# Kernel tuning notes

Measured on AMD Instinct MI355X. Metric: run time of the kernel, lower is better.

Reference implementation:

```python
import jax, jax.numpy as jnp
import numpy as np

N_NODES, NUM_FEAT, EMB, HID, N_CLASSES, N_EDGES = 800, 111, 32, 200, 15, 8000
ALPHA = 0.5   # DirGNNConv default mixing
EPS = 1e-5    # LayerNorm eps


def _pade_coeffs(deg=5):
    # [5/5] Pade approximant of sqrt(1 - x) (as in FastDifferentiableMatSqrt)
    K = 2 * deg + 1
    b = np.zeros(K); b[0] = 1.0
    for k in range(1, K):
        b[k] = b[k - 1] * (0.5 - (k - 1)) / k
    c = b * ((-1.0) ** np.arange(K))  # Taylor coeffs of sqrt(1-x)
    A = np.empty((deg, deg))
    for i in range(deg):
        for j in range(1, deg + 1):
            A[i, j - 1] = c[deg + 1 + i - j]
    q = np.concatenate([[1.0], np.linalg.solve(A, -c[deg + 1:])])
    p = np.array([sum(q[j] * c[k - j] for j in range(min(k, deg) + 1)) for k in range(deg + 1)])
    return p.astype(np.float32), q.astype(np.float32)

PADE_P, PADE_Q = _pade_coeffs()


def _mpa_impl(A):
    # matrix square root via Pade approximant (MPA forward)
    normA = jnp.sqrt(jnp.sum(A * A))
    I = jnp.eye(A.shape[0], dtype=A.dtype)
    p_app = I - A / normA
    p_hat = p_app
    p_sqrt = PADE_P[0] * I
    q_sqrt = PADE_Q[0] * I
    for i in range(5):
        p_sqrt = p_sqrt + PADE_P[i + 1] * p_hat
        q_sqrt = q_sqrt + PADE_Q[i + 1] * p_hat
        p_hat = p_hat @ p_app
    return jnp.linalg.solve(q_sqrt, p_sqrt) * jnp.sqrt(normA)


@jax.custom_vjp
def mpa_lya(A):
    return _mpa_impl(A)


def _mpa_fwd(A):
    S = _mpa_impl(A)
    return S, (S, jnp.sqrt(jnp.sum(A * A)))


def _mpa_bwd(res, g):
    # iterative Lyapunov solver backward (8 coupled Newton-Schulz iterations)
    S, normA = res
    I = jnp.eye(S.shape[0], dtype=S.dtype)
    b = S / jnp.sqrt(normA)
    c = g / jnp.sqrt(normA)
    for _ in range(8):
        b2 = b @ b
        c = 0.5 * (c @ (3.0 * I - b2) - b2 @ c + b @ (c @ b))
        b = 0.5 * (b @ (3.0 * I - b2))
    return (0.5 * c,)

mpa_lya.defvjp(_mpa_fwd, _mpa_bwd)


def gcn_sparse(m, ei, n):
    # GCNConv(normalize=False): out[dst] = sum_{(src,dst) in E} (x @ W)[src]
    return jax.ops.segment_sum(m[ei[0]], ei[1], num_segments=n)


def hetero_layer_sparse(h, eis, W, b):
    # W: [3(in,out,root), 4 edge types, Fin, Fout]; HeteroConv aggr='sum'
    n = h.shape[0]
    out = jnp.zeros((n, W.shape[-1]), h.dtype)
    for e, ei in enumerate(eis):
        x_in = gcn_sparse(h @ W[0, e], ei, n) + b[0, e]
        x_out = gcn_sparse(h @ W[1, e], ei[::-1], n) + b[1, e]  # flipped edges
        out = out + ALPHA * x_out + (1.0 - ALPHA) * x_in + h @ W[2, e] + b[2, e]
    return out


def hetero_layer_dense(h, masks, W, b):
    # masks: [4, N, N] binary adjacency (src, dst); dense equivalent of scatter
    out = jnp.zeros((h.shape[0], W.shape[-1]), h.dtype)
    for e in range(masks.shape[0]):
        x_in = masks[e].T @ (h @ W[0, e]) + b[0, e]
        x_out = masks[e] @ (h @ W[1, e]) + b[1, e]
        out = out + ALPHA * x_out + (1.0 - ALPHA) * x_in + h @ W[2, e] + b[2, e]
    return out


def graph_layernorm(h, wb):
    # PyG LayerNorm mode='graph', single graph: normalize over all nodes+feats
    mu = jnp.mean(h)
    var = jnp.mean((h - mu) ** 2)
    return (h - mu) / jnp.sqrt(var + EPS) * wb[0] + wb[1]


def hetero_gnn(h, layer_fn, graph, W1, b1, W2, b2, ln):
    h = graph_layernorm(layer_fn(h, graph, W1, b1), ln[0])
    return graph_layernorm(layer_fn(h, graph, W2, b2), ln[1])


def pairwise_S(z, lin_W, lin_b, iu, ju):
    n = z.shape[0]
    M = (z[iu] - z[ju]) ** 2                        # [N(N+1)/2, HID]
    mg = jax.nn.sigmoid(M @ lin_W + lin_b)[:, 0]    # upper-tri entries, row-major
    tri = jnp.zeros((n, n), z.dtype).at[iu, ju].set(mg)
    return mpa_lya(tri)


def model_forward(x_note, embed_W, embed_b, g1_l1_W, g1_l1_b, g1_l2_W, g1_l2_b, g1_ln,
                  g2_l1_W, g2_l1_b, g2_l2_W, g2_l2_b, g2_ln, lin_W, lin_b, clf_W, clf_b,
                  eis, batch):
    n = x_note.shape[0]
    iu, ju = np.triu_indices(n)
    h = x_note @ embed_W + embed_b                   # [N, 32]
    z0 = hetero_gnn(h, hetero_layer_sparse, eis, g1_l1_W, g1_l1_b, g1_l2_W, g1_l2_b, g1_ln)
    S1 = pairwise_S(z0, lin_W, lin_b, iu, ju)
    A0 = jnp.stack([jnp.zeros((n, n), h.dtype).at[ei[0], ei[1]].set(1.0) for ei in eis])
    h = S1 @ h
    # adj_to_coord(nonzero) only keeps the binary pattern of S1 @ A @ S1
    mask1 = jnp.stack([((S1 @ A0[e]) @ S1 != 0).astype(h.dtype) for e in range(4)])
    z1 = hetero_gnn(h, hetero_layer_dense, mask1, g2_l1_W, g2_l1_b, g2_l2_W, g2_l2_b, g2_ln)
    S2 = pairwise_S(z1, lin_W, lin_b, iu, ju)
    h = S2 @ h
    mask2 = jnp.stack([((S2 @ mask1[e]) @ S2 != 0).astype(h.dtype) for e in range(4)])
    z2 = hetero_gnn(h, hetero_layer_dense, mask2, g2_l1_W, g2_l1_b, g2_l2_W, g2_l2_b, g2_ln)
    counts = jax.ops.segment_sum(jnp.ones((n,), z2.dtype), batch, num_segments=1)
    x2 = jax.ops.segment_sum(z2, batch, num_segments=1) / counts[:, None]  # global_mean_pool
    logits = x2 @ clf_W + clf_b
    return x2, jax.nn.log_softmax(logits, axis=-1), S1, S2


def setup_inputs() -> dict:
    key = jax.random.key(0)
    ks = jax.random.split(key, 14)
    N, F, E, H, NC, NE = N_NODES, NUM_FEAT, EMB, HID, N_CLASSES, N_EDGES
    def w(k, shape, fan_in):
        return (jax.random.normal(k, shape, jnp.float32) / np.sqrt(fan_in)).astype(jnp.float32)
    ln = jnp.broadcast_to(jnp.stack([jnp.ones(H, jnp.float32), jnp.zeros(H, jnp.float32)]), (2, 2, H)) + 0.0
    return dict(
        x_note=jax.random.normal(ks[0], (N, F), jnp.float32),
        embed_W=w(ks[1], (F, E), F), embed_b=jnp.zeros((E,), jnp.float32),
        g1_l1_W=w(ks[2], (3, 4, E, H), E), g1_l1_b=jnp.zeros((3, 4, H), jnp.float32),
        g1_l2_W=w(ks[3], (3, 4, H, H), H), g1_l2_b=jnp.zeros((3, 4, H), jnp.float32),
        g1_ln=ln,
        g2_l1_W=w(ks[4], (3, 4, E, H), E), g2_l1_b=jnp.zeros((3, 4, H), jnp.float32),
        g2_l2_W=w(ks[5], (3, 4, H, H), H), g2_l2_b=jnp.zeros((3, 4, H), jnp.float32),
        g2_ln=ln,
        lin_W=w(ks[6], (H, 1), H), lin_b=jnp.zeros((1,), jnp.float32),
        clf_W=w(ks[7], (H, NC), H), clf_b=jnp.zeros((NC,), jnp.float32),
        ei_forward=jax.random.randint(ks[8], (2, NE), 0, N, jnp.int32),
        ei_onset=jax.random.randint(ks[9], (2, NE), 0, N, jnp.int32),
        ei_sustain=jax.random.randint(ks[10], (2, NE), 0, N, jnp.int32),
        ei_rest=jax.random.randint(ks[11], (2, NE), 0, N, jnp.int32),
        batch=jnp.zeros((N,), jnp.int32),
    )


def reference(x_note, embed_W, embed_b, g1_l1_W, g1_l1_b, g1_l2_W, g1_l2_b, g1_ln,
              g2_l1_W, g2_l1_b, g2_l2_W, g2_l2_b, g2_ln, lin_W, lin_b, clf_W, clf_b,
              ei_forward, ei_onset, ei_sustain, ei_rest, batch):
    eis = (ei_forward, ei_onset, ei_sustain, ei_rest)
    return model_forward(x_note, embed_W, embed_b, g1_l1_W, g1_l1_b, g1_l2_W, g1_l2_b, g1_ln,
                         g2_l1_W, g2_l1_b, g2_l2_W, g2_l2_b, g2_ln, lin_W, lin_b, clf_W, clf_b,
                         eis, batch)
```

## Files before the change

### kernel.cpp

```cpp
#include <hip/hip_runtime.h>
#include <hip/hip_bf16.h>
#include <math.h>
#include <stdio.h>

static constexpr int   kN  = 800;
static constexpr int   kF  = 111;
static constexpr int   kE  = 32;
static constexpr int   kH  = 200;
static constexpr int   kNC = 15;
static constexpr int   kNE = 8000;
static constexpr long  kNN = (long)kN*kN;
static constexpr long  kNH = (long)kN*kH;
static constexpr float kAl  = 0.5f;
static constexpr float kEps = 1e-5f;
static constexpr int   kGB  = (int)((kNH+255)/256);
static constexpr int   kDB  = 50;

typedef unsigned short u16;
typedef __attribute__((ext_vector_type(8))) short short8;
typedef __attribute__((ext_vector_type(4))) float f32x4;

__device__ __forceinline__ u16 f2bf(float v){
  __hip_bfloat16 b = __float2bfloat16(v);
  return *reinterpret_cast<u16*>(&b);
}
__device__ __forceinline__ float bf2f(u16 h){
  unsigned int u = ((unsigned int)h) << 16;
  float f; __builtin_memcpy(&f, &u, 4);
  return f;
}

enum { EPI_NONE=0, EPI_BIAS=1, EPI_SCALE=4, EPI_ACC=6 };

template<bool TRANSA, bool TRIUA, bool TRIUB, int EPI, bool LNA>
__global__ __launch_bounds__(256)
void gemm_kernel(const float* __restrict__ A, int lda,
                 const float* __restrict__ B, int ldb,
                 float* __restrict__ C, int ldc,
                 int M, int Ncl, int K,
                 long sA, long sB, long sC, float scale,
                 const float* __restrict__ bias, int kstep,
                 const double* __restrict__ scalp,
                 const float* __restrict__ lnw,
                 const double* __restrict__ lnpart, int lnnb)
{
  constexpr int TM=64, TN=64, TK=16;
  A += (long)blockIdx.z * sA;
  B += (long)blockIdx.z * sB;
  C += (long)blockIdx.z * sC;
  __shared__ float As[TK][TM+4];
  __shared__ float Bs[TK][TN+4];
  const int tid = threadIdx.x;
  const int tn4 = (tid & 15)*4, tm4 = (tid >> 4)*4;
  const int m0 = blockIdx.x * TM, n0 = blockIdx.y * TN;
  float acc[4][4] = {};
  float mu = 0.f, rsf = 1.f;
  if (LNA){
    __shared__ double lnS[256], lnQ[256];
    double s=0.0, q=0.0;
    for (int i=tid; i<lnnb; i+=256){ s += lnpart[2*i]; q += lnpart[2*i+1]; }
    lnS[tid]=s; lnQ[tid]=q;
    __syncthreads();
    for (int h=128; h>0; h>>=1){
      if (tid < h){ lnS[tid]+=lnS[tid+h]; lnQ[tid]+=lnQ[tid+h]; }
      __syncthreads();
    }
    double m = lnS[0]/(double)kNH;
    double var = lnQ[0]/(double)kNH - m*m;
    mu = (float)m;
    rsf = rsqrtf((float)var + kEps);
    __syncthreads();
  }
  const int kbase = kstep ? (int)blockIdx.z * kstep : 0;
  int k0 = TRIUA ? max(m0 - kbase, 0) : 0;
  int kEnd = TRIUB ? min(K, n0 + TN - kbase) : K;
  const bool skip = (k0 >= kEnd);
  if (skip && EPI == EPI_ACC) return;
  if (!skip) {
    float ar[4], br[4];
    auto loadT = [&](int kk0, float* arr, float* brr){
      #pragma unroll
      for (int u=0; u<4; ++u){
        int idx = tid + 256*u;
        float av = 0.f;
        if (!TRANSA) {
          int m = idx >> 4, ka = idx & 15;
          int gm = m0+m, gk = kk0+ka;
          if (gm < M && gk < K){
            av = A[(long)gm*lda + gk];
            if (LNA) av = (av - mu)*(rsf*lnw[gk]) + lnw[kH + gk];
          }
        } else {
          int ka = idx >> 6, m = idx & 63;
          int gm = m0+m, gk = kk0+ka;
          if (gm < M && gk < K){
            av = A[(long)gk*lda + gm];
            if (LNA) av = (av - mu)*(rsf*lnw[gk]) + lnw[kH + gk];
          }
        }
        int kb = idx >> 6, nb = idx & 63;
        int gk = kk0+kb, gn = n0+nb;
        arr[u] = av;
        brr[u] = (gk < K && gn < Ncl) ? B[(long)gk*ldb + gn] : 0.f;
      }
    };
    auto storeT = [&](const float* arr, const float* brr){
      #pragma unroll
      for (int u=0; u<4; ++u){
        int idx = tid + 256*u;
        if (!TRANSA){ int m = idx>>4, ka = idx&15; As[ka][m] = arr[u]; }
        else        { int ka = idx>>6, m = idx&63; As[ka][m] = arr[u]; }
        int kb = idx>>6, nb = idx&63;
        Bs[kb][nb] = brr[u];
      }
    };
    loadT(k0, ar, br);
    for (;;){
      __syncthreads();
      storeT(ar, br);
      __syncthreads();
      int kn = k0 + TK;
      bool more = kn < kEnd;
      if (more) loadT(kn, ar, br);
      #pragma unroll
      for (int kk=0; kk<TK; ++kk) {
        float a[4], b[4];
        #pragma unroll
        for (int u=0;u<4;++u){ a[u]=As[kk][tm4+u]; b[u]=Bs[kk][tn4+u]; }
        #pragma unroll
        for (int i=0;i<4;++i)
          #pragma unroll
          for (int j=0;j<4;++j)
            acc[i][j] = fmaf(a[i], b[j], acc[i][j]);
      }
      if (!more) break;
      k0 = kn;
    }
  }
  float sc = scale;
  if (EPI == EPI_ACC && scalp) sc *= (float)sqrt(sqrt(scalp[0]));
  #pragma unroll
  for (int i=0;i<4;++i) {
    int gm = m0 + tm4 + i;
    if (gm >= M) continue;
    #pragma unroll
    for (int j=0;j<4;++j) {
      int gn = n0 + tn4 + j;
      if (gn >= Ncl) continue;
      float v = acc[i][j];
      long off = (long)gm*ldc + gn;
      if (EPI == EPI_BIAS)       C[off] = v + bias[gn];
      else if (EPI == EPI_SCALE) C[off] = scale*v;
      else if (EPI == EPI_ACC)   unsafeAtomicAdd(&C[off], sc*v);
      else                       C[off] = v;
    }
  }
}

template<bool TRANSA, bool TRIUA, bool TRIUB, int EPI, bool LNA = false>
static inline void launch_gemm(hipStream_t st,
                               const float* A, int lda, const float* B, int ldb,
                               float* C, int ldc, int M, int Ncl, int K, int batch,
                               long sA, long sB, long sC, float scale,
                               const float* bias = nullptr, int kstep = 0,
                               const double* scalp = nullptr,
                               const float* lnw = nullptr,
                               const double* lnpart = nullptr, int lnnb = 0)
{
  dim3 grid((M+63)/64, (Ncl+63)/64, batch);
  gemm_kernel<TRANSA,TRIUA,TRIUB,EPI,LNA><<<grid, 256, 0, st>>>(
      A,lda,B,ldb,C,ldc,M,Ncl,K,sA,sB,sC,scale,bias,kstep,scalp,lnw,lnpart,lnnb);
}

__global__ __launch_bounds__(256)
void bgemm2_kernel(const u16* __restrict__ Ah, const u16* __restrict__ Al,
                   const u16* __restrict__ Bh, const u16* __restrict__ Bl,
                   float* __restrict__ C, float* __restrict__ C2,
                   u16* __restrict__ Oh, u16* __restrict__ Ol,
                   float p0, float p1)
{
  constexpr int TM=64, TN=64, BK=32;
  __shared__ u16 Ash[TM][40], Asl[TM][40], Bsh[TN][40], Bsl[TN][40];
  const int tid = threadIdx.x;
  const int m0 = blockIdx.x*TM, n0 = blockIdx.y*TN;
  const int w = tid>>6, lane = tid&63;
  const int wm = (w&1)*32, wn = (w>>1)*32;
  const int quad = lane>>4, lm = lane&15;
  f32x4 acc00={}, acc01={}, acc10={}, acc11={};
  const bool skip = (m0 > n0 + TN - 1);
  int k0 = m0;
  const int kEnd = min(kN, n0+TN);
  const int ar = tid>>2, ac = (tid&3)*8;
  if (!skip){
    uint4 avh, avl, bvh, bvl;
    auto loadT = [&](int kk0){
      avh = {0,0,0,0}; avl = {0,0,0,0}; bvh = {0,0,0,0}; bvl = {0,0,0,0};
      int gk = kk0 + ac;
      if (m0+ar < kN && gk < kN){
        avh = *(const uint4*)(Ah + (long)(m0+ar)*kN + gk);
        avl = *(const uint4*)(Al + (long)(m0+ar)*kN + gk);
      }
      if (n0+ar < kN && gk < kN){
        bvh = *(const uint4*)(Bh + (long)(n0+ar)*kN + gk);
        bvl = *(const uint4*)(Bl + (long)(n0+ar)*kN + gk);
      }
    };
    loadT(k0);
    for (;;){
      __syncthreads();
      *(uint4*)&Ash[ar][ac] = avh; *(uint4*)&Asl[ar][ac] = avl;
      *(uint4*)&Bsh[ar][ac] = bvh; *(uint4*)&Bsl[ar][ac] = bvl;
      __syncthreads();
      int kn = k0 + BK;
      bool more = kn < kEnd;
      if (more) loadT(kn);
      short8 a0h = *(const short8*)&Ash[wm+lm][quad*8];
      short8 a1h = *(const short8*)&Ash[wm+16+lm][quad*8];
      short8 a0l = *(const short8*)&Asl[wm+lm][quad*8];
      short8 a1l = *(const short8*)&Asl[wm+16+lm][quad*8];
      short8 b0h = *(const short8*)&Bsh[wn+lm][quad*8];
      short8 b1h = *(const short8*)&Bsh[wn+16+lm][quad*8];
      short8 b0l = *(const short8*)&Bsl[wn+lm][quad*8];
      short8 b1l = *(const short8*)&Bsl[wn+16+lm][quad*8];
      acc00 = __builtin_amdgcn_mfma_f32_16x16x32_bf16(a0h,b0h,acc00,0,0,0);
      acc00 = __builtin_amdgcn_mfma_f32_16x16x32_bf16(a0h,b0l,acc00,0,0,0);
      acc00 = __builtin_amdgcn_mfma_f32_16x16x32_bf16(a0l,b0h,acc00,0,0,0);
      acc01 = __builtin_amdgcn_mfma_f32_16x16x32_bf16(a0h,b1h,acc01,0,0,0);
      acc01 = __builtin_amdgcn_mfma_f32_16x16x32_bf16(a0h,b1l,acc01,0,0,0);
      acc01 = __builtin_amdgcn_mfma_f32_16x16x32_bf16(a0l,b1h,acc01,0,0,0);
      acc10 = __builtin_amdgcn_mfma_f32_16x16x32_bf16(a1h,b0h,acc10,0,0,0);
      acc10 = __builtin_amdgcn_mfma_f32_16x16x32_bf16(a1h,b0l,acc10,0,0,0);
      acc10 = __builtin_amdgcn_mfma_f32_16x16x32_bf16(a1l,b0h,acc10,0,0,0);
      acc11 = __builtin_amdgcn_mfma_f32_16x16x32_bf16(a1h,b1h,acc11,0,0,0);
      acc11 = __builtin_amdgcn_mfma_f32_16x16x32_bf16(a1h,b1l,acc11,0,0,0);
      acc11 = __builtin_amdgcn_mfma_f32_16x16x32_bf16(a1l,b1h,acc11,0,0,0);
      if (!more) break;
      k0 = kn;
    }
  }
  f32x4 accs[2][2] = {{acc00, acc01},{acc10, acc11}};
  #pragma unroll
  for (int ti=0; ti<2; ++ti){
    #pragma unroll
    for (int tj=0; tj<2; ++tj){
      #pragma unroll
      for (int r=0; r<4; ++r){
        int gm = m0 + wm + ti*16 + quad*4 + r;
        int gn = n0 + wn + tj*16 + lm;
        if (gm >= kN || gn >= kN) continue;
        float v = accs[ti][tj][r];
        long off = (long)gm*kN + gn;
        C[off]  += p0*v;
        C2[off] += p1*v;
        u16 h = f2bf(v);
        Oh[off] = h;
        Ol[off] = f2bf(v - bf2f(h));
      }
    }
  }
}

__global__ __launch_bounds__(256)
void ln_pair_prep_kernel(const float* __restrict__ tnh, const double* __restrict__ part,
                         int nb, const float* __restrict__ ln, const float* __restrict__ linW,
                         u16* __restrict__ zwh, u16* __restrict__ zwl,
                         u16* __restrict__ zzh, u16* __restrict__ zzl,
                         float* __restrict__ avec)
{
  __shared__ double ss[256], qq[256];
  __shared__ float ared[256];
  const int n = blockIdx.x, t = threadIdx.x;
  double s=0.0, q=0.0;
  for (int i=t; i<nb; i+=256){ s += part[2*i]; q += part[2*i+1]; }
  ss[t]=s; qq[t]=q;
  __syncthreads();
  for (int h=128; h>0; h>>=1){
    if (t < h){ ss[t]+=ss[t+h]; qq[t]+=qq[t+h]; }
    __syncthreads();
  }
  double m = ss[0]/(double)kNH;
  const float mu = (float)m;
  const float rs = rsqrtf((float)(qq[0]/(double)kNH - m*m) + kEps);
  float acc = 0.f;
  if (t < kH){
    float z = (tnh[(long)n*kH + t] - mu)*(rs*ln[t]) + ln[kH + t];
    float wv = linW[t];
    float zw = wv*z;
    long off = (long)n*kH + t;
    u16 h1 = f2bf(zw);
    zwh[off] = h1; zwl[off] = f2bf(zw - bf2f(h1));
    u16 h2 = f2bf(z);
    zzh[off] = h2; zzl[off] = f2bf(z - bf2f(h2));
    acc = zw*z;
  }
  ared[t] = acc;
  __syncthreads();
  for (int h=128; h>0; h>>=1){
    if (t < h) ared[t] += ared[t+h];
    __syncthreads();
  }
  if (t == 0) avec[n] = ared[0];
}

__global__ __launch_bounds__(256)
void bgemm_pair_kernel(const u16* __restrict__ Ah, const u16* __restrict__ Al,
                       const u16* __restrict__ Bh, const u16* __restrict__ Bl,
                       const float* __restrict__ avec, const float* __restrict__ linb,
                       float* __restrict__ tri, double* __restrict__ frob2)
{
  constexpr int TM=64, TN=64, BK=32, KK=kH;
  __shared__ u16 Ash[TM][40], Asl[TM][40], Bsh[TN][40], Bsl[TN][40];
  __shared__ float red[256];
  const int tid = threadIdx.x;
  const int m0 = blockIdx.x*TM, n0 = blockIdx.y*TN;
  if (m0 > n0 + TN - 1){
    for (int idx = tid; idx < TM*TN; idx += 256){
      int r = idx >> 6, c = idx & 63;
      int gm = m0 + r, gn = n0 + c;
      if (gm < kN && gn < kN) tri[(long)gm*kN + gn] = 0.f;
    }
    return;
  }
  const int w = tid>>6, lane = tid&63;
  const int wm = (w&1)*32, wn = (w>>1)*32;
  const int quad = lane>>4, lm = lane&15;
  f32x4 acc00={}, acc01={}, acc10={}, acc11={};
  const int ar = tid>>2, ac = (tid&3)*8;
  for (int k0 = 0; k0 < KK; k0 += BK){
    uint4 avh={0,0,0,0}, avl={0,0,0,0}, bvh={0,0,0,0}, bvl={0,0,0,0};
    int gk = k0 + ac;
    if (m0+ar < kN && gk < KK){
      avh = *(const uint4*)(Ah + (long)(m0+ar)*KK + gk);
      avl = *(const uint4*)(Al + (long)(m0+ar)*KK + gk);
    }
    if (n0+ar < kN && gk < KK){
      bvh = *(const uint4*)(Bh + (long)(n0+ar)*KK + gk);
      bvl = *(const uint4*)(Bl + (long)(n0+ar)*KK + gk);
    }
    __syncthreads();
    *(uint4*)&Ash[ar][ac] = avh; *(uint4*)&Asl[ar][ac] = avl;
    *(uint4*)&Bsh[ar][ac] = bvh; *(uint4*)&Bsl[ar][ac] = bvl;
    __syncthreads();
    short8 a0h = *(const short8*)&Ash[wm+lm][quad*8];
    short8 a1h = *(const short8*)&Ash[wm+16+lm][quad*8];
    short8 a0l = *(const short8*)&Asl[wm+lm][quad*8];
    short8 a1l = *(const short8*)&Asl[wm+16+lm][quad*8];
    short8 b0h = *(const short8*)&Bsh[wn+lm][quad*8];
    short8 b1h = *(const short8*)&Bsh[wn+16+lm][quad*8];
    short8 b0l = *(const short8*)&Bsl[wn+lm][quad*8];
    short8 b1l = *(const short8*)&Bsl[wn+16+lm][quad*8];
    acc00 = __builtin_amdgcn_mfma_f32_16x16x32_bf16(a0h,b0h,acc00,0,0,0);
    acc00 = __builtin_amdgcn_mfma_f32_16x16x32_bf16(a0h,b0l,acc00,0,0,0);
    acc00 = __builtin_amdgcn_mfma_f32_16x16x32_bf16(a0l,b0h,acc00,0,0,0);
    acc01 = __builtin_amdgcn_mfma_f32_16x16x32_bf16(a0h,b1h,acc01,0,0,0);
    acc01 = __builtin_amdgcn_mfma_f32_16x16x32_bf16(a0h,b1l,acc01,0,0,0);
    acc01 = __builtin_amdgcn_mfma_f32_16x16x32_bf16(a0l,b1h,acc01,0,0,0);
    acc10 = __builtin_amdgcn_mfma_f32_16x16x32_bf16(a1h,b0h,acc10,0,0,0);
    acc10 = __builtin_amdgcn_mfma_f32_16x16x32_bf16(a1h,b0l,acc10,0,0,0);
    acc10 = __builtin_amdgcn_mfma_f32_16x16x32_bf16(a1l,b0h,acc10,0,0,0);
    acc11 = __builtin_amdgcn_mfma_f32_16x16x32_bf16(a1h,b1h,acc11,0,0,0);
    acc11 = __builtin_amdgcn_mfma_f32_16x16x32_bf16(a1h,b1l,acc11,0,0,0);
    acc11 = __builtin_amdgcn_mfma_f32_16x16x32_bf16(a1l,b1h,acc11,0,0,0);
  }
  const float lb = linb[0];
  float r2 = 0.f;
  f32x4 accs[2][2] = {{acc00, acc01},{acc10, acc11}};
  #pragma unroll
  for (int ti=0; ti<2; ++ti){
    #pragma unroll
    for (int tj=0; tj<2; ++tj){
      #pragma unroll
      for (int r=0; r<4; ++r){
        int gm = m0 + wm + ti*16 + quad*4 + r;
        int gn = n0 + wn + tj*16 + lm;
        if (gm >= kN || gn >= kN) continue;
        float t = 0.f;
        if (gm <= gn){
          float marg = avec[gm] + avec[gn] - 2.f*accs[ti][tj][r] + lb;
          t = 1.f/(1.f + expf(-marg));
        }
        tri[(long)gm*kN + gn] = t;
        r2 += t*t;
      }
    }
  }
  red[tid] = r2;
  __syncthreads();
  for (int h=128; h>0; h>>=1){
    if (tid < h) red[tid] += red[tid+h];
    __syncthreads();
  }
  if (tid == 0) unsafeAtomicAdd(frob2, (double)red[0]);
}

__global__ __launch_bounds__(256)
void pade_both_kernel(const float* __restrict__ tri, const double* __restrict__ frob2,
                      u16* __restrict__ ph, u16* __restrict__ pl,
                      u16* __restrict__ th, u16* __restrict__ tl,
                      float* __restrict__ psq, float* __restrict__ qsq,
                      float P0, float P1, float Q0, float Q1)
{
  __shared__ float t[32][33];
  const float rn = (float)(1.0 / sqrt(frob2[0]));
  int r0 = blockIdx.y*32, c0 = blockIdx.x*32;
  int tr = threadIdx.x>>5, tc = threadIdx.x&31;
  for (int i=tr; i<32; i+=8){
    int r = r0+i, c = c0+tc;
    float eye = (r==c) ? 1.f : 0.f;
    float pa = eye - tri[(long)r*kN + c]*rn;
    t[i][tc] = pa;
    long off = (long)r*kN + c;
    psq[off] = P0*eye + P1*pa;
    qsq[off] = Q0*eye + Q1*pa;
    u16 h = f2bf(pa);
    ph[off] = h;
    pl[off] = f2bf(pa - bf2f(h));
  }
  __syncthreads();
  for (int i=tr; i<32; i+=8){
    int c = c0+i, r = r0+tc;
    float v = t[tc][i];
    u16 h = f2bf(v);
    th[(long)c*kN + r] = h;
    tl[(long)c*kN + r] = f2bf(v - bf2f(h));
  }
}

__global__ __launch_bounds__(256)
void copy_scale_kernel(const float* __restrict__ src, const double* __restrict__ frob2,
                       float* __restrict__ dst)
{
  const float fac = (float)sqrt(sqrt(frob2[0]));
  long i = (long)blockIdx.x*256 + threadIdx.x;
  if (i < kNN) __builtin_nontemporal_store(src[i]*fac, &dst[i]);
}

__global__ void edge_count_kernel(const int* __restrict__ e0, const int* __restrict__ e1,
                                  const int* __restrict__ e2, const int* __restrict__ e3,
                                  int* __restrict__ cnt){
  const int* eis[4] = {e0,e1,e2,e3};
  const int e = blockIdx.y;
  const int* ei = eis[e];
  int j = blockIdx.x*256 + threadIdx.x;
  if (j >= kNE) return;
  int s = ei[j], d = ei[kNE + j];
  atomicAdd(&cnt[e*kN + d], 1);
  atomicAdd(&cnt[(4+e)*kN + s], 1);
}

__global__ void csr_scan_kernel(const int* __restrict__ cnt, int* __restrict__ offs,
                                int* __restrict__ cur){
  const int l = blockIdx.x;
  if (threadIdx.x != 0) return;
  int acc = 0;
  for (int i = 0; i < kN; ++i){
    offs[l*(kN+1) + i] = acc;
    cur[l*kN + i] = acc;
    acc += cnt[l*kN + i];
  }
  offs[l*(kN+1) + kN] = acc;
}

__global__ void edge_fill_kernel(const int* __restrict__ e0, const int* __restrict__ e1,
                                 const int* __restrict__ e2, const int* __restrict__ e3,
                                 int* __restrict__ cur, int* __restrict__ adj){
  const int* eis[4] = {e0,e1,e2,e3};
  const int e = blockIdx.y;
  const int* ei = eis[e];
  int j = blockIdx.x*256 + threadIdx.x;
  if (j >= kNE) return;
  int s = ei[j], d = ei[kNE + j];
  int p = atomicAdd(&cur[e*kN + d], 1);
  adj[(long)e*kNE + p] = s;
  int q = atomicAdd(&cur[(4+e)*kN + s], 1);
  adj[(long)(4+e)*kNE + q] = d;
}

__global__ __launch_bounds__(256)
void gather_sparse_kernel(const float* __restrict__ Y, const int* __restrict__ offs,
                          const int* __restrict__ adj, const float* __restrict__ bsum,
                          float* __restrict__ tnh, double* __restrict__ part){
  __shared__ double ss[256], qq[256];
  const int n = blockIdx.x;
  const int f = threadIdx.x;
  double sp = 0.0, qp = 0.0;
  float acc = 0.f;
  if (f < kH){
    #pragma unroll
    for (int l = 0; l < 8; ++l){
      const float* Yp = Y + (long)l*kNH;
      int b = offs[l*(kN+1) + n], e2 = offs[l*(kN+1) + n + 1];
      for (int idx = b; idx < e2; ++idx){
        int m = adj[(long)l*kNE + idx];
        acc += Yp[(long)m*kH + f];
      }
    }
    float t = Y[(long)8*kNH + (long)n*kH + f] + bsum[f] + 0.5f*acc;
    tnh[(long)n*kH + f] = t;
    sp = t; qp = (double)t*t;
  }
  ss[threadIdx.x]=sp; qq[threadIdx.x]=qp;
  __syncthreads();
  for (int hh=128; hh>0; hh>>=1){
    if ((int)threadIdx.x < hh){ ss[threadIdx.x]+=ss[threadIdx.x+hh]; qq[threadIdx.x]+=qq[threadIdx.x+hh]; }
    __syncthreads();
  }
  if (threadIdx.x==0){ part[2*blockIdx.x]=ss[0]; part[2*blockIdx.x+1]=qq[0]; }
}

__global__ void edge_gmax_kernel(const int* __restrict__ e0, const int* __restrict__ e1,
                                 const int* __restrict__ e2, const int* __restrict__ e3,
                                 int* __restrict__ g){
  const int* eis[4] = {e0,e1,e2,e3};
  const int e = blockIdx.y;
  const int* ei = eis[e];
  int j = blockIdx.x*256 + threadIdx.x;
  if (j >= kNE) return;
  int s = ei[j], d = ei[kNE + j];
  atomicMax(&g[e*kN + d], s);
}

__global__ __launch_bounds__(256)
void scan_gh_kernel(int* __restrict__ g, int* __restrict__ h){
  __shared__ int gs[kN];
  const int e = blockIdx.x;
  for (int i = threadIdx.x; i < kN; i += 256) gs[i] = g[e*kN + i];
  __syncthreads();
  if (threadIdx.x == 0){
    int m = -1;
    for (int i = 0; i < kN; ++i){ m = max(m, gs[i]); gs[i] = m; }
  }
  __syncthreads();
  for (int i = threadIdx.x; i < kN; i += 256) g[e*kN + i] = gs[i];
  for (int d = threadIdx.x; d < kN; d += 256){
    int lo = 0, hi = kN;
    while (lo < hi){ int mid = (lo+hi)>>1; if (gs[mid] >= d) hi = mid; else lo = mid+1; }
    h[e*kN + d] = lo;
  }
}

__global__ __launch_bounds__(256)
void scan_msg_kernel(float* __restrict__ Y){
  const int plane = blockIdx.x;
  const int f = threadIdx.x;
  if (f >= kH) return;
  float* P = Y + (long)plane*kNH + f;
  float acc = 0.f;
  if (plane < 4){
    for (int n = 0; n < kN; n += 4){
      float v0 = P[(long)(n+0)*kH], v1 = P[(long)(n+1)*kH];
      float v2 = P[(long)(n+2)*kH], v3 = P[(long)(n+3)*kH];
      acc += v0; P[(long)(n+0)*kH] = acc;
      acc += v1; P[(long)(n+1)*kH] = acc;
      acc += v2; P[(long)(n+2)*kH] = acc;
      acc += v3; P[(long)(n+3)*kH] = acc;
    }
  } else {
    for (int n = kN-1; n >= 0; n -= 4){
      float v0 = P[(long)(n-0)*kH], v1 = P[(long)(n-1)*kH];
      float v2 = P[(long)(n-2)*kH], v3 = P[(long)(n-3)*kH];
      acc += v0; P[(long)(n-0)*kH] = acc;
      acc += v1; P[(long)(n-1)*kH] = acc;
      acc += v2; P[(long)(n-2)*kH] = acc;
      acc += v3; P[(long)(n-3)*kH] = acc;
    }
  }
}

__global__ __launch_bounds__(256)
void gather_dense_kernel(const float* __restrict__ Y, const int* __restrict__ g,
                         const int* __restrict__ h, const float* __restrict__ bsum,
                         float* __restrict__ tnh, double* __restrict__ part){
  __shared__ double ss[256], qq[256];
  long idx = (long)blockIdx.x*256 + threadIdx.x;
  double s = 0.0, q = 0.0;
  if (idx < kNH){
    int n = (int)(idx / kH), f = (int)(idx % kH);
    float v = 0.f;
    #pragma unroll
    for (int e = 0; e < 4; ++e){
      int gi = g[e*kN + n];
      if (gi >= 0) v += Y[(long)e*kNH + (long)gi*kH + f];
      int hi = h[e*kN + n];
      if (hi < kN) v += Y[(long)(4+e)*kNH + (long)hi*kH + f];
    }
    float t = Y[(long)8*kNH + idx] + bsum[f] + 0.5f*v;
    tnh[idx] = t;
    s = t; q = (double)t*t;
  }
  ss[threadIdx.x]=s; qq[threadIdx.x]=q;
  __syncthreads();
  for (int hh=128; hh>0; hh>>=1){
    if ((int)threadIdx.x < hh){ ss[threadIdx.x]+=ss[threadIdx.x+hh]; qq[threadIdx.x]+=qq[threadIdx.x+hh]; }
    __syncthreads();
  }
  if (threadIdx.x==0){ part[2*blockIdx.x]=ss[0]; part[2*blockIdx.x+1]=qq[0]; }
}

__global__ void sum_root_kernel(const float* __restrict__ W, const float* __restrict__ b,
                                int K, float* __restrict__ Wr, float* __restrict__ bsum){
  int idx = blockIdx.x*256 + threadIdx.x;
  int tot = K*kH;
  if (idx < tot){
    float v = 0.f;
    #pragma unroll
    for (int e=0;e<4;++e) v += W[(long)(8+e)*tot + idx];
    Wr[idx] = v;
  }
  if (idx < kH){
    float v = 0.f;
    #pragma unroll
    for (int e=0;e<4;++e)
      v += (1.f-kAl)*b[(0*4+e)*kH + idx] + kAl*b[(1*4+e)*kH + idx] + b[(2*4+e)*kH + idx];
    bsum[idx] = v;
  }
}

__global__ __launch_bounds__(64)
void invdiag_kernel(const float* __restrict__ U, float* __restrict__ W){
  __shared__ float Us[kDB][kDB+1];
  __shared__ float Xs[kDB][kDB+1];
  const int base = blockIdx.x * kDB;
  const int tid = threadIdx.x;
  for (int idx = tid; idx < kDB*kDB; idx += 64){
    int r = idx / kDB, c = idx % kDB;
    Us[r][c] = U[(long)(base+r)*kN + base + c];
  }
  __syncthreads();
  const int c = tid;
  for (int i = kDB-1; i >= 0; --i){
    if (c < kDB){
      float x;
      if (c < i) x = 0.f;
      else {
        float s = 0.f;
        for (int k = i+1; k < kDB; ++k) s = fmaf(Us[i][k], Xs[k][c], s);
        x = (((c==i)?1.f:0.f) - s) / Us[i][i];
      }
      Xs[i][c] = x;
    }
    __syncthreads();
  }
  for (int idx = tid; idx < kDB*kDB; idx += 64){
    int r = idx / kDB, cc = idx % kDB;
    W[(long)(base+r)*kN + base + cc] = Xs[r][cc];
  }
}

template<int S>
__global__ __launch_bounds__(256)
void merge_fused_kernel(const float* __restrict__ U, float* __restrict__ W){
  __shared__ float Us[S][S+1];
  __shared__ float Wb[S][S+1];
  __shared__ float T[S][S+1];
  const long base = (long)blockIdx.x * (2*S) * (kN+1);
  const int tid = threadIdx.x;
  for (int idx = tid; idx < S*S; idx += 256){
    int r = idx / S, c = idx % S;
    Us[r][c] = U[base + (long)r*kN + S + c];
    Wb[r][c] = W[base + (long)(S+r)*kN + S + c];
  }
  __syncthreads();
  for (int idx = tid; idx < S*S; idx += 256){
    int r = idx / S, c = idx % S;
    float s = 0.f;
    for (int k = 0; k <= c; ++k) s = fmaf(Us[r][k], Wb[k][c], s);
    T[r][c] = s;
  }
  __syncthreads();
  for (int idx = tid; idx < S*S; idx += 256){
    int r = idx / S, c = idx % S;
    Us[r][c] = W[base + (long)r*kN + c];
  }
  __syncthreads();
  for (int idx = tid; idx < S*S; idx += 256){
    int r = idx / S, c = idx % S;
    float s = 0.f;
    for (int k = r; k < S; ++k) s = fmaf(Us[r][k], T[k][c], s);
    W[base + (long)r*kN + S + c] = -s;
  }
}

__global__ __launch_bounds__(256)
void pool_head_kernel(const float* __restrict__ z2raw, const double* __restrict__ part, int nb,
                      const float* __restrict__ ln,
                      const float* __restrict__ W, const float* __restrict__ b,
                      float* __restrict__ out){
  __shared__ double sred[256], qred[256];
  __shared__ float x2[kH];
  __shared__ float lg[kNC];
  int t = threadIdx.x;
  double s=0.0, q=0.0;
  for (int i=t; i<nb; i+=256){ s += part[2*i]; q += part[2*i+1]; }
  sred[t]=s; qred[t]=q;
  __syncthreads();
  for (int hh=128; hh>0; hh>>=1){
    if (t < hh){ sred[t]+=sred[t+hh]; qred[t]+=qred[t+hh]; }
    __syncthreads();
  }
  const float mu = (float)(sred[0] / (double)kNH);
  const float rs = rsqrtf((float)(qred[0]/(double)kNH - (sred[0]/(double)kNH)*(sred[0]/(double)kNH)) + kEps);
  if (t < kH){
    float sc = rs*ln[t], of = ln[kH+t];
    float sum = 0.f;
    for (int n = 0; n < kN; ++n) sum += (z2raw[(long)n*kH + t] - mu)*sc + of;
    float v = sum * (1.f/(float)kN);
    x2[t] = v;
    out[t] = v;
  }
  __syncthreads();
  if (t < kNC){
    float sv = b[t];
    for (int f = 0; f < kH; ++f) sv = fmaf(x2[f], W[f*kNC + t], sv);
    lg[t] = sv;
  }
  __syncthreads();
  if (t == 0){
    float m = -1e30f;
    for (int c=0;c<kNC;++c) m = fmaxf(m, lg[c]);
    float se = 0.f;
    for (int c=0;c<kNC;++c) se += expf(lg[c]-m);
    float lse = m + logf(se);
    for (int c=0;c<kNC;++c) out[kH + c] = lg[c]-lse;
  }
}

static void pade_coeffs(float* P, float* Q){
  double b[11]; b[0] = 1.0;
  for (int k=1;k<11;++k) b[k] = b[k-1]*(0.5-(k-1))/k;
  double c[11];
  for (int k=0;k<11;++k) c[k] = b[k]*((k&1)?-1.0:1.0);
  double A[5][5], rhs[5];
  for (int i=0;i<5;++i){ for (int j=0;j<5;++j) A[i][j] = c[5+i-j]; rhs[i] = -c[6+i]; }
  for (int col=0; col<5; ++col){
    int p = col;
    for (int r=col+1;r<5;++r) if (fabs(A[r][col]) > fabs(A[p][col])) p = r;
    if (p != col){
      for (int j=0;j<5;++j){ double t=A[col][j]; A[col][j]=A[p][j]; A[p][j]=t; }
      double t=rhs[col]; rhs[col]=rhs[p]; rhs[p]=t;
    }
    for (int r=col+1;r<5;++r){
      double f = A[r][col]/A[col][col];
      for (int j=col;j<5;++j) A[r][j] -= f*A[col][j];
      rhs[r] -= f*rhs[col];
    }
  }
  double q[6]; q[0] = 1.0;
  for (int r=4;r>=0;--r){
    double s = rhs[r];
    for (int j=r+1;j<5;++j) s -= A[r][j]*q[1+j];
    q[1+r] = s/A[r][r];
  }
  double p[6];
  for (int k=0;k<6;++k){
    double s = 0.0; int jm = k<5?k:5;
    for (int j=0;j<=jm;++j) s += q[j]*c[k-j];
    p[k] = s;
  }
  for (int k=0;k<6;++k){ P[k]=(float)p[k]; Q[k]=(float)q[k]; }
}

extern "C" void kernel_launch(void* const* d_in, const int* in_sizes, int n_in,
                              void* d_out, int out_size, void* d_ws, size_t ws_size,
                              hipStream_t stream)
{
  const float* x_note = (const float*)d_in[0];
  const float* embW   = (const float*)d_in[1];
  const float* embB   = (const float*)d_in[2];
  const float* g1w1   = (const float*)d_in[3];
  const float* g1b1   = (const float*)d_in[4];
  const float* g1w2   = (const float*)d_in[5];
  const float* g1b2   = (const float*)d_in[6];
  const float* g1ln   = (const float*)d_in[7];
  const float* g2w1   = (const float*)d_in[8];
  const float* g2b1   = (const float*)d_in[9];
  const float* g2w2   = (const float*)d_in[10];
  const float* g2b2   = (const float*)d_in[11];
  const float* g2ln   = (const float*)d_in[12];
  const float* linW   = (const float*)d_in[13];
  const float* linb   = (const float*)d_in[14];
  const float* clfW   = (const float*)d_in[15];
  const float* clfb   = (const float*)d_in[16];
  const int*  e0     = (const int*)d_in[17];
  const int*  e1     = (const int*)d_in[18];
  const int*  e2     = (const int*)d_in[19];
  const int*  e3     = (const int*)d_in[20];
  float* out = (float*)d_out;

  constexpr long o_h0   = 4096;
  constexpr long o_h1   = o_h0   + (long)kN*kE;
  constexpr long o_h2   = o_h1   + (long)kN*kE;
  constexpr long o_tnh  = o_h2   + (long)kN*kE;
  constexpr long o_pp   = o_tnh  + kNH;
  constexpr long o_av   = o_pp   + 2*kNH;
  constexpr long o_big  = o_av   + kN;
  constexpr long o_tri  = o_big  + 4*kNN;
  constexpr long o_sacc = o_tri  + kNN;
  constexpr long o_winv = o_sacc + kNN;
  constexpr long o_psq  = o_winv + kNN;
  constexpr long o_qsq  = o_psq  + kNN;
  constexpr long o_g    = o_qsq  + kNN;
  constexpr long o_hh   = o_g    + 4*kN;
  constexpr long o_wc1  = o_hh   + 4*kN;
  constexpr long o_wc2  = o_wc1  + 9L*kE*kH;
  constexpr long o_wc3  = o_wc2  + 9L*kH*kH;
  constexpr long o_wc4  = o_wc3  + 9L*kE*kH;
  constexpr long o_bs   = o_wc4  + 9L*kH*kH;
  constexpr long o_cnt  = o_bs   + 4*kH;
  constexpr long o_offs = o_cnt  + 8*kN;
  constexpr long o_cur  = o_offs + 8*(kN+1);
  constexpr long o_adj  = o_cur  + 8*kN;
  constexpr long o_end  = o_adj  + 8*(long)kNE;

  if (ws_size < (size_t)o_end*sizeof(float) || out_size < 215 + 2*(int)kNN || n_in < 21){
    fprintf(stderr, "kernel_launch guard: ws=%zu need=%zu out=%d need=%d n_in=%d\n",
            ws_size, (size_t)o_end*sizeof(float), out_size, (int)(215+2*kNN), n_in);
    hipMemsetAsync(d_out, 0, (size_t)out_size*sizeof(float), stream);
    return;
  }

  float* ws = (float*)d_ws;
  double* scald = (double*)d_ws;
  double* partd = (double*)((char*)d_ws + 512);
  float *h0=ws+o_h0, *h1=ws+o_h1, *h2=ws+o_h2, *tnh=ws+o_tnh,
        *big=ws+o_big, *tri=ws+o_tri, *Sacc=ws+o_sacc, *winv=ws+o_winv,
        *psq=ws+o_psq, *qsq=ws+o_qsq;
  u16* zwh = (u16*)(ws + o_pp);
  u16* zwl = zwh + kNH;
  u16* zzh = zwl + kNH;
  u16* zzl = zzh + kNH;
  float* avec = ws + o_av;
  int* gArr = (int*)(ws + o_g);
  int* hArr = (int*)(ws + o_hh);
  float *wc1=ws+o_wc1, *wc2=ws+o_wc2, *wc3=ws+o_wc3, *wc4=ws+o_wc4, *bs=ws+o_bs;
  int* cntA = (int*)(ws + o_cnt);
  int* offsA= (int*)(ws + o_offs);
  int* curA = (int*)(ws + o_cur);
  int* adjA = (int*)(ws + o_adj);
  u16* papp_h = (u16*)big;
  u16* papp_l = papp_h + kNN;
  u16* pT_h   = papp_l + kNN;
  u16* pT_l   = pT_h + kNN;
  u16* pwA_h  = pT_l + kNN;
  u16* pwA_l  = pwA_h + kNN;
  u16* pwB_h  = pwA_l + kNN;
  u16* pwB_l  = pwB_h + kNN;

  float P[6], Q[6];
  pade_coeffs(P, Q);

  auto eg = [](long n){ return dim3((unsigned)((n+255)/256)); };

  auto layer_gemm = [&](const float* hin, int K, const float* wcat,
                        const float* lnp, int nb){
    if (lnp)
      launch_gemm<false,false,false,EPI_NONE,true>(stream, hin, K, wcat, kH, big, kH,
          kN, kH, K, 9, 0, (long)K*kH, kNH, 0.f, nullptr, 0, nullptr, lnp, partd, nb);
    else
      launch_gemm<false,false,false,EPI_NONE>(stream, hin, K, wcat, kH, big, kH,
          kN, kH, K, 9, 0, (long)K*kH, kNH, 0.f);
  };
  auto sparse_layer = [&](const float* hin, int K, const float* wcat, const float* bsum,
                          const float* lnp, int nb){
    layer_gemm(hin, K, wcat, lnp, nb);
    gather_sparse_kernel<<<dim3(kN),256,0,stream>>>(big, offsA, adjA, bsum, tnh, partd);
  };
  auto dense_layer = [&](const float* hin, int K, const float* wcat, const float* bsum,
                         const float* lnp, int nb){
    layer_gemm(hin, K, wcat, lnp, nb);
    scan_msg_kernel<<<8,256,0,stream>>>(big);
    gather_dense_kernel<<<kGB,256,0,stream>>>(big, gArr, hArr, bsum, tnh, partd);
  };
  auto blocked_trsm = [&](){
    hipMemsetAsync(winv, 0, (size_t)kNN*sizeof(float), stream);
    invdiag_kernel<<<dim3(kN/kDB),64,0,stream>>>(qsq, winv);
    merge_fused_kernel<50><<<dim3(kN/100),256,0,stream>>>(qsq, winv);
    {
      int s = 100, npairs = 4;
      long step = (long)2*s*kN + 2*s;
      launch_gemm<false,false,true,EPI_NONE>(stream,
          qsq + s, kN, winv + (long)s*kN + s, kN, tri, s,
          s, s, s, npairs, step, step, (long)s*s, 0.f);
      launch_gemm<false,true,false,EPI_SCALE>(stream,
          winv, kN, tri, s, winv + s, kN,
          s, s, s, npairs, step, (long)s*s, step, -1.f);
    }
    {
      int s = 200, npairs = 2;
      long step = (long)2*s*kN + 2*s;
      launch_gemm<false,false,true,EPI_NONE>(stream,
          qsq + s, kN, winv + (long)s*kN + s, kN, tri, s,
          s, s, s, npairs, step, step, (long)s*s, 0.f);
      launch_gemm<false,true,false,EPI_SCALE>(stream,
          winv, kN, tri, s, winv + s, kN,
          s, s, s, npairs, step, (long)s*s, step, -1.f);
    }
    {
      hipMemsetAsync(tri, 0, (size_t)400*400*sizeof(float), stream);
      launch_gemm<false,false,true,EPI_ACC>(stream,
          qsq + 400, kN, winv + (long)400*kN + 400, kN, tri, 400,
          400, 400, 100, 4, 100, (long)100*kN, 0, 1.f, nullptr, 100);
      launch_gemm<false,true,false,EPI_ACC>(stream,
          winv, kN, tri, 400, winv + 400, kN,
          400, 400, 100, 4, 100, (long)100*400, 0, -1.f, nullptr, 100);
    }
    hipMemsetAsync(Sacc, 0, (size_t)kNN*sizeof(float), stream);
    launch_gemm<false,true,true,EPI_ACC>(stream,
        winv, kN, psq, kN, Sacc, kN, kN, kN, 100, 8,
        100, (long)100*kN, 0, 1.f, nullptr, 100);
  };
  auto run_pair_mpa = [&](int nb, const float* lnp, float* SoutDst){
    hipMemsetAsync((char*)d_ws + 24, 0, 8, stream);
    ln_pair_prep_kernel<<<dim3(kN),256,0,stream>>>(tnh, partd, nb, lnp, linW,
                                                   zwh, zwl, zzh, zzl, avec);
    bgemm_pair_kernel<<<dim3(13,13),256,0,stream>>>(zwh, zwl, zzh, zzl, avec, linb,
                                                    tri, scald+3);
    pade_both_kernel<<<dim3(25,25),256,0,stream>>>(tri, scald+3, papp_h, papp_l, pT_h, pT_l,
                                                   psq, qsq, P[0],P[1],Q[0],Q[1]);
    dim3 g13(13,13,1);
    bgemm2_kernel<<<g13,256,0,stream>>>(papp_h,papp_l, pT_h,pT_l, psq,qsq, pwA_h,pwA_l, P[2],Q[2]);
    bgemm2_kernel<<<g13,256,0,stream>>>(pwA_h,pwA_l,  pT_h,pT_l, psq,qsq, pwB_h,pwB_l, P[3],Q[3]);
    bgemm2_kernel<<<g13,256,0,stream>>>(pwB_h,pwB_l,  pT_h,pT_l, psq,qsq, pwA_h,pwA_l, P[4],Q[4]);
    bgemm2_kernel<<<g13,256,0,stream>>>(pwA_h,pwA_l,  pT_h,pT_l, psq,qsq, pwB_h,pwB_l, P[5],Q[5]);
    blocked_trsm();
    copy_scale_kernel<<<eg(kNN),256,0,stream>>>(Sacc, scald+3, SoutDst);
  };
  auto s_times_h = [&](const float* hin, float* hout){
    hipMemsetAsync(hout, 0, (size_t)kN*kE*sizeof(float), stream);
    launch_gemm<false,true,false,EPI_ACC>(stream,
        Sacc, kN, hin, kE, hout, kE, kN, kE, 100, 8,
        100, (long)100*kE, 0, 1.f, nullptr, 100, scald+3);
  };

  float* S1f = out + 215;
  float* S2f = out + 215 + kNN;

  hipMemsetAsync(gArr, 0xFF, (size_t)(4*kN)*sizeof(int), stream);
  edge_gmax_kernel<<<dim3((kNE+255)/256,4),256,0,stream>>>(e0,e1,e2,e3, gArr);
  scan_gh_kernel<<<4,256,0,stream>>>(gArr, hArr);
  hipMemsetAsync(cntA, 0, (size_t)(8*kN)*sizeof(int), stream);
  edge_count_kernel<<<dim3((kNE+255)/256,4),256,0,stream>>>(e0,e1,e2,e3, cntA);
  csr_scan_kernel<<<8,64,0,stream>>>(cntA, offsA, curA);
  edge_fill_kernel<<<dim3((kNE+255)/256,4),256,0,stream>>>(e0,e1,e2,e3, curA, adjA);
  hipMemcpyAsync(wc1, g1w1, 8L*kE*kH*sizeof(float), hipMemcpyDeviceToDevice, stream);
  hipMemcpyAsync(wc2, g1w2, 8L*kH*kH*sizeof(float), hipMemcpyDeviceToDevice, stream);
  hipMemcpyAsync(wc3, g2w1, 8L*kE*kH*sizeof(float), hipMemcpyDeviceToDevice, stream);
  hipMemcpyAsync(wc4, g2w2, 8L*kH*kH*sizeof(float), hipMemcpyDeviceToDevice, stream);
  sum_root_kernel<<<eg((long)kE*kH),256,0,stream>>>(g1w1, g1b1, kE, wc1 + 8L*kE*kH, bs);
  sum_root_kernel<<<eg((long)kH*kH),256,0,stream>>>(g1w2, g1b2, kH, wc2 + 8L*kH*kH, bs+kH);
  sum_root_kernel<<<eg((long)kE*kH),256,0,stream>>>(g2w1, g2b1, kE, wc3 + 8L*kE*kH, bs+2*kH);
  sum_root_kernel<<<eg((long)kH*kH),256,0,stream>>>(g2w2, g2b2, kH, wc4 + 8L*kH*kH, bs+3*kH);

  launch_gemm<false,false,false,EPI_BIAS>(stream, x_note, kF, embW, kE, h0, kE, kN, kE, kF, 1,
                                          0,0,0, 0.f, embB);

  sparse_layer(h0,  kE, wc1, bs,      nullptr, 0);
  sparse_layer(tnh, kH, wc2, bs+kH,   g1ln, kN);

  run_pair_mpa(kN, g1ln + 2*kH, S1f);

  s_times_h(h0, h1);

  dense_layer(h1,  kE, wc3, bs+2*kH, nullptr, 0);
  dense_layer(tnh, kH, wc4, bs+3*kH, g2ln, kGB);

  run_pair_mpa(kGB, g2ln + 2*kH, S2f);

  s_times_h(h1, h2);

  dense_layer(h2,  kE, wc3, bs+2*kH, nullptr, 0);
  dense_layer(tnh, kH, wc4, bs+3*kH, g2ln, kGB);

  pool_head_kernel<<<dim3(1),256,0,stream>>>(tnh, partd, kGB, g2ln + 2*kH, clfW, clfb, out);
}
```

Baseline: 1.134 ms.

## Parallelize dense-layer prefix scan into chunks and split final pooling column sum

The serial 800-row prefix scan (8 blocks) is replaced by a chunked scan over 16 chunks per plane, storing per-chunk totals. The gather kernel then adds the preceding or following chunk totals on the fly. The single-block pooling head no longer walks all 800 rows itself. A 50-block column-sum kernel produces partials, and LayerNorm is applied to the mean algebraically. This targets serial-latency bottlenecks, at the cost of extra loops in the gather and an additional launch.

```diff
diff --git a/kernel.cpp b/kernel.cpp
--- a/kernel.cpp
+++ b/kernel.cpp
@@ -15,6 +15,8 @@
 static constexpr float kEps = 1e-5f;
 static constexpr int   kGB  = (int)((kNH+255)/256);
 static constexpr int   kDB  = 50;
+static constexpr int   kCH  = 50;
+static constexpr int   kNCHK= kN/kCH;
 
 typedef unsigned short u16;
 typedef __attribute__((ext_vector_type(8))) short short8;
@@ -540,36 +542,41 @@
 }
 
 __global__ __launch_bounds__(256)
-void scan_msg_kernel(float* __restrict__ Y){
-  const int plane = blockIdx.x;
+void scan_chunk_kernel(float* __restrict__ Y, float* __restrict__ Tot){
+  const int plane = blockIdx.y;
+  const int chunk = blockIdx.x;
   const int f = threadIdx.x;
   if (f >= kH) return;
-  float* P = Y + (long)plane*kNH + f;
+  float* P = Y + (long)plane*kNH + (long)chunk*kCH*kH + f;
   float acc = 0.f;
   if (plane < 4){
-    for (int n = 0; n < kN; n += 4){
-      float v0 = P[(long)(n+0)*kH], v1 = P[(long)(n+1)*kH];
-      float v2 = P[(long)(n+2)*kH], v3 = P[(long)(n+3)*kH];
-      acc += v0; P[(long)(n+0)*kH] = acc;
-      acc += v1; P[(long)(n+1)*kH] = acc;
-      acc += v2; P[(long)(n+2)*kH] = acc;
-      acc += v3; P[(long)(n+3)*kH] = acc;
+    for (int i0 = 0; i0 < kCH; i0 += 5){
+      float v0 = P[(long)(i0+0)*kH], v1 = P[(long)(i0+1)*kH], v2 = P[(long)(i0+2)*kH],
+            v3 = P[(long)(i0+3)*kH], v4 = P[(long)(i0+4)*kH];
+      acc += v0; P[(long)(i0+0)*kH] = acc;
+      acc += v1; P[(long)(i0+1)*kH] = acc;
+      acc += v2; P[(long)(i0+2)*kH] = acc;
+      acc += v3; P[(long)(i0+3)*kH] = acc;
+      acc += v4; P[(long)(i0+4)*kH] = acc;
     }
   } else {
-    for (int n = kN-1; n >= 0; n -= 4){
-      float v0 = P[(long)(n-0)*kH], v1 = P[(long)(n-1)*kH];
-      float v2 = P[(long)(n-2)*kH], v3 = P[(long)(n-3)*kH];
-      acc += v0; P[(long)(n-0)*kH] = acc;
-      acc += v1; P[(long)(n-1)*kH] = acc;
-      acc += v2; P[(long)(n-2)*kH] = acc;
-      acc += v3; P[(long)(n-3)*kH] = acc;
-    }
-  }
+    for (int i0 = kCH-1; i0 >= 4; i0 -= 5){
+      float v0 = P[(long)(i0-0)*kH], v1 = P[(long)(i0-1)*kH], v2 = P[(long)(i0-2)*kH],
+            v3 = P[(long)(i0-3)*kH], v4 = P[(long)(i0-4)*kH];
+      acc += v0; P[(long)(i0-0)*kH] = acc;
+      acc += v1; P[(long)(i0-1)*kH] = acc;
+      acc += v2; P[(long)(i0-2)*kH] = acc;
+      acc += v3; P[(long)(i0-3)*kH] = acc;
+      acc += v4; P[(long)(i0-4)*kH] = acc;
+    }
+  }
+  Tot[((long)plane*kNCHK + chunk)*kH + f] = acc;
 }
 
 __global__ __launch_bounds__(256)
 void gather_dense_kernel(const float* __restrict__ Y, const int* __restrict__ g,
                          const int* __restrict__ h, const float* __restrict__ bsum,
+                         const float* __restrict__ Tot,
                          float* __restrict__ tnh, double* __restrict__ part){
   __shared__ double ss[256], qq[256];
   long idx = (long)blockIdx.x*256 + threadIdx.x;
@@ -580,9 +587,19 @@
     #pragma unroll
     for (int e = 0; e < 4; ++e){
       int gi = g[e*kN + n];
-      if (gi >= 0) v += Y[(long)e*kNH + (long)gi*kH + f];
+      if (gi >= 0){
+        v += Y[(long)e*kNH + (long)gi*kH + f];
+        int cg = (int)((unsigned)gi / (unsigned)kCH);
+        const float* T = Tot + (long)e*kNCHK*kH + f;
+        for (int cc = 0; cc < cg; ++cc) v += T[(long)cc*kH];
+      }
       int hi = h[e*kN + n];
-      if (hi < kN) v += Y[(long)(4+e)*kNH + (long)hi*kH + f];
+      if (hi < kN){
+        v += Y[(long)(4+e)*kNH + (long)hi*kH + f];
+        int ch = (int)((unsigned)hi / (unsigned)kCH);
+        const float* T = Tot + (long)(4+e)*kNCHK*kH + f;
+        for (int cc = ch+1; cc < kNCHK; ++cc) v += T[(long)cc*kH];
+      }
     }
     float t = Y[(long)8*kNH + idx] + bsum[f] + 0.5f*v;
     tnh[idx] = t;
@@ -682,7 +699,19 @@
 }
 
 __global__ __launch_bounds__(256)
-void pool_head_kernel(const float* __restrict__ z2raw, const double* __restrict__ part, int nb,
+void colsum_kernel(const float* __restrict__ tnh, float* __restrict__ colpart){
+  const int b = blockIdx.x;
+  const int f = threadIdx.x;
+  if (f >= kH) return;
+  const float* P = tnh + (long)b*16*kH + f;
+  float acc = 0.f;
+  #pragma unroll
+  for (int i = 0; i < 16; ++i) acc += P[(long)i*kH];
+  colpart[(long)b*kH + f] = acc;
+}
+
+__global__ __launch_bounds__(256)
+void pool_head_kernel(const float* __restrict__ colpart, const double* __restrict__ part, int nb,
                       const float* __restrict__ ln,
                       const float* __restrict__ W, const float* __restrict__ b,
                       float* __restrict__ out){
@@ -701,10 +730,9 @@
   const float mu = (float)(sred[0] / (double)kNH);
   const float rs = rsqrtf((float)(qred[0]/(double)kNH - (sred[0]/(double)kNH)*(sred[0]/(double)kNH)) + kEps);
   if (t < kH){
-    float sc = rs*ln[t], of = ln[kH+t];
     float sum = 0.f;
-    for (int n = 0; n < kN; ++n) sum += (z2raw[(long)n*kH + t] - mu)*sc + of;
-    float v = sum * (1.f/(float)kN);
+    for (int bb = 0; bb < 50; ++bb) sum += colpart[(long)bb*kH + t];
+    float v = (sum * (1.f/(float)kN) - mu)*(rs*ln[t]) + ln[kH+t];
     x2[t] = v;
     out[t] = v;
   }
@@ -845,6 +873,8 @@
   u16* pwA_l  = pwA_h + kNN;
   u16* pwB_h  = pwA_l + kNN;
   u16* pwB_l  = pwB_h + kNN;
+  float* totbuf  = big + (long)9*kNH;
+  float* colpart = totbuf + (long)8*kNCHK*kH;
 
   float P[6], Q[6];
   pade_coeffs(P, Q);
@@ -868,8 +898,8 @@
   auto dense_layer = [&](const float* hin, int K, const float* wcat, const float* bsum,
                          const float* lnp, int nb){
     layer_gemm(hin, K, wcat, lnp, nb);
-    scan_msg_kernel<<<8,256,0,stream>>>(big);
-    gather_dense_kernel<<<kGB,256,0,stream>>>(big, gArr, hArr, bsum, tnh, partd);
+    scan_chunk_kernel<<<dim3(kNCHK,8),256,0,stream>>>(big, totbuf);
+    gather_dense_kernel<<<kGB,256,0,stream>>>(big, gArr, hArr, bsum, totbuf, tnh, partd);
   };
   auto blocked_trsm = [&](){
     hipMemsetAsync(winv, 0, (size_t)kNN*sizeof(float), stream);
@@ -971,5 +1001,6 @@
   dense_layer(h2,  kE, wc3, bs+2*kH, nullptr, 0);
   dense_layer(tnh, kH, wc4, bs+3*kH, g2ln, kGB);
 
-  pool_head_kernel<<<dim3(1),256,0,stream>>>(tnh, partd, kGB, g2ln + 2*kH, clfW, clfb, out);
-}
+  colsum_kernel<<<dim3(50),256,0,stream>>>(tnh, colpart);
+  pool_head_kernel<<<dim3(1),256,0,stream>>>(colpart, partd, kGB, g2ln + 2*kH, clfW, clfb, out);
+}
```

Result: faster. 1.068 ms (-5.8%).
